# Optimization experiments

Measured on AMD Instinct MI355X. Metric: run time of the kernel, lower is better.

## Reference

```python
import jax, jax.numpy as jnp
import numpy as np

HEADS = 16
HEAD_DIM = 64
DIM = HEADS * HEAD_DIM          # 1024
TEXT_LEN = 226
N_CONCEPTS = 8
FRAMES = 4
PATCHES = 16 * 24               # H*W per latent frame
IMG_LEN = FRAMES * PATCHES      # 1536
TIME_DIM = 512
FF_DIM = 4 * DIM
TOPK_HEADS = 4                  # imap_sep_topk
LN_EPS = 1e-5
QK_EPS = 1e-6


def _layer_norm(x, w, b, eps):
    mu = jnp.mean(x, -1, keepdims=True)
    var = jnp.var(x, -1, keepdims=True)
    return (x - mu) * jax.lax.rsqrt(var + eps) * w + b


def _norm_zero(h, e, temb, lw, lb, nw, nb):
    # CogVideoXLayerNormZero: adaLN shift/scale/gate for hidden and encoder streams
    s = jax.nn.silu(temb) @ lw + lb                      # [B, 6*DIM]
    shift, scale, gate, e_shift, e_scale, e_gate = jnp.split(s, 6, axis=1)
    hn = _layer_norm(h, nw, nb, LN_EPS) * (1 + scale)[:, None] + shift[:, None]
    en = _layer_norm(e, nw, nb, LN_EPS) * (1 + e_scale)[:, None] + e_shift[:, None]
    return hn, en, gate[:, None], e_gate[:, None]


def _heads(x):
    B, S, _ = x.shape
    return x.reshape(B, S, HEADS, HEAD_DIM).transpose(0, 2, 1, 3)


def _rope(x, cos, sin):
    # diffusers apply_rotary_emb, use_real_unbind_dim=-1
    xr = x.reshape(*x.shape[:-1], HEAD_DIM // 2, 2)
    rot = jnp.stack([-xr[..., 1], xr[..., 0]], -1).reshape(x.shape)
    return x * cos + rot * sin


def _sdpa(q, k, v):
    s = jnp.einsum('bhqd,bhkd->bhqk', q, k) * (1.0 / np.sqrt(HEAD_DIM))
    return jnp.einsum('bhqk,bhkd->bhqd', jax.nn.softmax(s, -1), v)


def _attention(norm_h, norm_e, norm_c, rope_cos, rope_sin,
               wq, wk, wv, nq_w, nq_b, nk_w, nk_b, wo, bo):
    B = norm_h.shape[0]
    hs = jnp.concatenate([norm_e, norm_h], axis=1)       # [B, T+P, DIM]
    q, k, v = _heads(hs @ wq), _heads(hs @ wk), _heads(hs @ wv)
    cq, ck, cv = _heads(norm_c @ wq), _heads(norm_c @ wk), _heads(norm_c @ wv)
    q = _layer_norm(q, nq_w, nq_b, QK_EPS); cq = _layer_norm(cq, nq_w, nq_b, QK_EPS)
    k = _layer_norm(k, nk_w, nk_b, QK_EPS); ck = _layer_norm(ck, nk_w, nk_b, QK_EPS)
    q = q.at[:, :, TEXT_LEN:].set(_rope(q[:, :, TEXT_LEN:], rope_cos, rope_sin))
    k = k.at[:, :, TEXT_LEN:].set(_rope(k[:, :, TEXT_LEN:], rope_cos, rope_sin))

    attn_out = _sdpa(q, k, v)                            # [B,H,S,D]
    img_hidden = attn_out[:, :, TEXT_LEN:]               # [B,H,IMG_LEN,D]

    # select_head (reconstructed): per-head spread of image-token activations, top-k heads
    head_score = jnp.std(jnp.mean(img_hidden[1], -1), -1)        # [H]
    _, sel_head_idx = jax.lax.top_k(head_score, TOPK_HEADS)

    iq, ik, iv = q[:, :, TEXT_LEN:], k[:, :, TEXT_LEN:], v[:, :, TEXT_LEN:]
    cat_q = jnp.concatenate([cq, iq], 2)
    cat_k = jnp.concatenate([ck, ik], 2)
    cat_v = jnp.concatenate([cv, iv], 2)
    concept_attn = _sdpa(cat_q, cat_k, cat_v)
    attn_concept = concept_attn[:, :, :N_CONCEPTS]       # [B,H,C,D]

    cross_maps = jnp.mean(jnp.einsum('hpd,hcd->hcp', iq[1], ck[1]), axis=0)
    concept_maps = jnp.sum(jnp.einsum('hcd,hpd->hcp', attn_concept[1], img_hidden[1]), axis=0)

    # select_visual_token (reconstructed): per (head, concept, frame) argmax patch of q.k sim
    text_key = ck[1]                                      # imap_qk_matching_target == 'concept'
    sim = jnp.einsum('hpd,htd->htp', iq[1], text_key).reshape(HEADS, N_CONCEPTS, FRAMES, PATCHES)
    sel_vis_idx = jnp.argmax(sim, axis=-1)                # [H,T,F]

    img_r = img_hidden[1].reshape(HEADS, FRAMES, PATCHES, HEAD_DIM)
    h_ix = jnp.arange(HEADS)[:, None, None]
    f_ix = jnp.arange(FRAMES)[None, None, :]
    sel_img = img_r[h_ix, f_ix, sel_vis_idx]              # [H,T,F,D] gather
    imap = jnp.einsum('htfd,hfpd->htfp', sel_img, img_r)
    imap = (imap - imap.mean(1, keepdims=True)) / (jnp.std(imap, axis=1, keepdims=True, ddof=1) + 1e-6)
    imap = imap.reshape(HEADS, N_CONCEPTS, FRAMES * PATCHES)
    sel_imap = jnp.mean(imap[sel_head_idx], axis=0)       # [T, F*P]
    imap_sum = jnp.sum(imap, axis=0)

    def merge(x):
        return x.transpose(0, 2, 1, 3).reshape(B, x.shape[2], DIM)

    out = merge(attn_out) @ wo + bo
    c_out = merge(attn_concept) @ wo + bo
    return out[:, TEXT_LEN:], out[:, :TEXT_LEN], c_out, sel_imap, imap_sum, concept_maps, cross_maps


def _ff(x, w1, b1, w2, b2):
    return jax.nn.gelu(x @ w1 + b1, approximate=True) @ w2 + b2


def _block(hidden_states, encoder_hidden_states, concept_hidden_states, temb,
           rope_cos, rope_sin,
           norm1_w, norm1_b, ln1_w, ln1_b, norm2_w, norm2_b, ln2_w, ln2_b,
           wq, wk, wv, nq_w, nq_b, nk_w, nk_b, wo, bo,
           ff_w1, ff_b1, ff_w2, ff_b2):
    h, e, c = hidden_states, encoder_hidden_states, concept_hidden_states
    nh, ne, g_msa, eg_msa = _norm_zero(h, e, temb, norm1_w, norm1_b, ln1_w, ln1_b)
    _, nc, _, cg_msa = _norm_zero(h, c, temb, norm1_w, norm1_b, ln1_w, ln1_b)

    a_h, a_e, a_c, sel_imap, imap, concept_maps, cross_maps = _attention(
        nh, ne, nc, rope_cos, rope_sin, wq, wk, wv, nq_w, nq_b, nk_w, nk_b, wo, bo)

    h = h + g_msa * a_h
    e = e + eg_msa * a_e
    c = c + cg_msa * a_c

    nh, ne, g_ff, eg_ff = _norm_zero(h, e, temb, norm2_w, norm2_b, ln2_w, ln2_b)
    _, nc, _, cg_ff = _norm_zero(h, c, temb, norm2_w, norm2_b, ln2_w, ln2_b)

    ff_out = _ff(jnp.concatenate([ne, nh], axis=1), ff_w1, ff_b1, ff_w2, ff_b2)
    ff_c = _ff(nc, ff_w1, ff_b1, ff_w2, ff_b2)
    h = h + g_ff * ff_out[:, TEXT_LEN:]
    e = e + eg_ff * ff_out[:, :TEXT_LEN]
    c = c + cg_ff * ff_c
    return h, e, c, sel_imap, imap, concept_maps, cross_maps


def setup_inputs():
    key = jax.random.key(0)
    ks = jax.random.split(key, 16)
    p = lambda i, shape: jax.random.normal(ks[i], shape, jnp.float32) * 0.02
    return dict(
        hidden_states=jax.random.normal(ks[0], (2, IMG_LEN, DIM), jnp.float32),
        encoder_hidden_states=jax.random.normal(ks[1], (2, TEXT_LEN, DIM), jnp.float32),
        concept_hidden_states=jax.random.normal(ks[2], (2, N_CONCEPTS, DIM), jnp.float32),
        temb=jax.random.normal(ks[3], (2, TIME_DIM), jnp.float32),
        rope_cos=jax.random.uniform(ks[4], (IMG_LEN, HEAD_DIM), jnp.float32),
        rope_sin=jax.random.uniform(ks[5], (IMG_LEN, HEAD_DIM), jnp.float32),
        norm1_w=p(6, (TIME_DIM, 6 * DIM)), norm1_b=jnp.zeros((6 * DIM,), jnp.float32),
        ln1_w=jnp.ones((DIM,), jnp.float32), ln1_b=jnp.zeros((DIM,), jnp.float32),
        norm2_w=p(7, (TIME_DIM, 6 * DIM)), norm2_b=jnp.zeros((6 * DIM,), jnp.float32),
        ln2_w=jnp.ones((DIM,), jnp.float32), ln2_b=jnp.zeros((DIM,), jnp.float32),
        wq=p(8, (DIM, DIM)), wk=p(9, (DIM, DIM)), wv=p(10, (DIM, DIM)),
        nq_w=jnp.ones((HEAD_DIM,), jnp.float32), nq_b=jnp.zeros((HEAD_DIM,), jnp.float32),
        nk_w=jnp.ones((HEAD_DIM,), jnp.float32), nk_b=jnp.zeros((HEAD_DIM,), jnp.float32),
        wo=p(11, (DIM, DIM)), bo=jnp.zeros((DIM,), jnp.float32),
        ff_w1=p(12, (DIM, FF_DIM)), ff_b1=jnp.zeros((FF_DIM,), jnp.float32),
        ff_w2=p(13, (FF_DIM, DIM)), ff_b2=jnp.zeros((DIM,), jnp.float32),
    )


def reference(hidden_states, encoder_hidden_states, concept_hidden_states, temb,
              rope_cos, rope_sin,
              norm1_w, norm1_b, ln1_w, ln1_b, norm2_w, norm2_b, ln2_w, ln2_b,
              wq, wk, wv, nq_w, nq_b, nk_w, nk_b, wo, bo,
              ff_w1, ff_b1, ff_w2, ff_b2):
    return _block(hidden_states, encoder_hidden_states, concept_hidden_states, temb,
                  rope_cos, rope_sin,
                  norm1_w, norm1_b, ln1_w, ln1_b, norm2_w, norm2_b, ln2_w, ln2_b,
                  wq, wk, wv, nq_w, nq_b, nk_w, nk_b, wo, bo,
                  ff_w1, ff_b1, ff_w2, ff_b2)
```

## Files before the change

kernel.cpp:

```cpp
#include <hip/hip_runtime.h>
#include <hip/hip_bf16.h>
#include <math.h>

#define B_ 2
#define HEADS_ 16
#define HD_ 64
#define DIM_ 1024
#define TEXT_ 226
#define NC_ 8
#define FRAMES_ 4
#define PATCHES_ 384
#define IMG_ 1536
#define S_MAIN 1762
#define S2_ 1770
#define TD_ 512
#define FF_ 4096
#define ROWS_ (B_*S2_)
#define VPAD_ 1792

#define OFF_S1   0L
#define OFF_S2   12288L
#define OFF_MISC 24576L
#define OFF_SIM  25600L
#define OFF_IMAP 222208L
#define OFF_AC   418816L
#define OFF_X    435200L
#define OFF_PROJ 4060160L
#define OFF_XN   7685120L
#define OFF_Q    11310080L
#define OFF_K    14935040L
#define OFF_V    18560000L
#define OFF_AO   22184960L
#define OFF_XNB  25809920L

#define O_H    0L
#define O_E    3145728L
#define O_C    3608576L
#define O_SELI 3624960L
#define O_ISUM 3637248L
#define O_CMAP 3649536L
#define O_XMAP 3661824L

typedef __bf16 bf16x8_t __attribute__((ext_vector_type(8)));
typedef float  f32x4_t  __attribute__((ext_vector_type(4)));

__device__ __forceinline__ unsigned int pack2bf(float a, float b) {
    unsigned short ua = __builtin_bit_cast(unsigned short, (__bf16)a);
    unsigned short ub = __builtin_bit_cast(unsigned short, (__bf16)b);
    return (unsigned int)ua | ((unsigned int)ub << 16);
}

__global__ __launch_bounds__(256) void k_silu_mod(
    const float* __restrict__ temb, const float* __restrict__ w1, const float* __restrict__ b1,
    const float* __restrict__ w2, const float* __restrict__ b2,
    float* __restrict__ s1, float* __restrict__ s2)
{
    int gout = blockIdx.x * 64 + (threadIdx.x & 63);
    int ks = threadIdx.x >> 6;
    int which = gout / 12288;
    int r = gout % 12288;
    int b = r / 6144, n = r % 6144;
    const float* w = which ? w2 : w1;
    const float* bb = which ? b2 : b1;
    const float* t = temb + b * TD_;
    float acc = 0.f;
    for (int k = ks*128; k < ks*128 + 128; ++k) {
        float tv = t[k];
        float sv = tv / (1.f + __expf(-tv));
        acc += sv * w[(long)k * 6144 + n];
    }
    __shared__ float red[256];
    red[threadIdx.x] = acc; __syncthreads();
    if (ks == 0) {
        int lt = threadIdx.x;
        float v = red[lt] + red[lt+64] + red[lt+128] + red[lt+192] + bb[n];
        (which ? s2 : s1)[b * 6144 + n] = v;
    }
}

__global__ __launch_bounds__(256) void k_tcvt(
    const float* __restrict__ src, unsigned short* __restrict__ dst, int K, int N)
{
    __shared__ float t[32][33];
    int n0 = blockIdx.x * 32, k0 = blockIdx.y * 32;
    int tx = threadIdx.x & 31, ty = threadIdx.x >> 5;
    #pragma unroll
    for (int i = 0; i < 4; ++i)
        t[ty + 8*i][tx] = src[(size_t)(k0 + ty + 8*i) * N + n0 + tx];
    __syncthreads();
    #pragma unroll
    for (int i = 0; i < 4; ++i) {
        float v = t[tx][ty + 8*i];
        dst[(size_t)(n0 + ty + 8*i) * K + k0 + tx] =
            __builtin_bit_cast(unsigned short, (__bf16)v);
    }
}

__global__ __launch_bounds__(256) void k_tcvt_qkv(
    const float* __restrict__ wq, const float* __restrict__ wk, const float* __restrict__ wv,
    unsigned short* __restrict__ dst)
{
    const float* src = (blockIdx.z == 0) ? wq : (blockIdx.z == 1) ? wk : wv;
    unsigned short* d = dst + (size_t)blockIdx.z * 1024 * 1024;
    __shared__ float t[32][33];
    int n0 = blockIdx.x * 32, k0 = blockIdx.y * 32;
    int tx = threadIdx.x & 31, ty = threadIdx.x >> 5;
    #pragma unroll
    for (int i = 0; i < 4; ++i)
        t[ty + 8*i][tx] = src[(size_t)(k0 + ty + 8*i) * 1024 + n0 + tx];
    __syncthreads();
    #pragma unroll
    for (int i = 0; i < 4; ++i) {
        float v = t[tx][ty + 8*i];
        d[(size_t)(n0 + ty + 8*i) * 1024 + k0 + tx] =
            __builtin_bit_cast(unsigned short, (__bf16)v);
    }
}

__global__ __launch_bounds__(256) void k_vtrans(
    const float* __restrict__ vh, unsigned short* __restrict__ vb)
{
    int bh = blockIdx.z;
    int d0 = blockIdx.y * 32;
    int s0 = blockIdx.x * 32;
    __shared__ float t[32][33];
    int tx = threadIdx.x & 31, ty = threadIdx.x >> 5;
    const float* src = vh + (size_t)bh * S2_ * 64;
    #pragma unroll
    for (int i = 0; i < 4; ++i) {
        int s = s0 + ty + 8*i; if (s >= S2_) s = S2_ - 1;
        t[ty + 8*i][tx] = src[(size_t)s*64 + d0 + tx];
    }
    __syncthreads();
    unsigned short* dst = vb + (size_t)bh * 64 * VPAD_;
    #pragma unroll
    for (int i = 0; i < 4; ++i) {
        int d = d0 + ty + 8*i;
        dst[(size_t)d * VPAD_ + s0 + tx] =
            __builtin_bit_cast(unsigned short, (__bf16)t[tx][ty + 8*i]);
    }
}

__global__ __launch_bounds__(256) void k_ln_mod(
    const float* pe, long bse, const float* ph, long bsh, const float* pc, long bsc,
    const float* __restrict__ smod, const float* __restrict__ lnw, const float* __restrict__ lnb,
    float* __restrict__ out, unsigned short* __restrict__ outb)
{
    long row = blockIdx.x;
    int b = (int)(row / S2_), s = (int)(row % S2_);
    const float* src; int shiftB, scaleB;
    if (s < TEXT_)       { src = pe + (long)b*bse + (long)s*DIM_;          shiftB = 3072; scaleB = 4096; }
    else if (s < S_MAIN) { src = ph + (long)b*bsh + (long)(s-TEXT_)*DIM_;  shiftB = 0;    scaleB = 1024; }
    else                 { src = pc + (long)b*bsc + (long)(s-S_MAIN)*DIM_; shiftB = 3072; scaleB = 4096; }
    int tid = threadIdx.x;
    int col = tid * 4;
    float4 x = *(const float4*)(src + col);
    float lsum = x.x + x.y + x.z + x.w;
    float lsq  = x.x*x.x + x.y*x.y + x.z*x.z + x.w*x.w;
    __shared__ float r1[256], r2[256];
    r1[tid] = lsum; r2[tid] = lsq; __syncthreads();
    for (int st = 128; st; st >>= 1) {
        if (tid < st) { r1[tid] += r1[tid+st]; r2[tid] += r2[tid+st]; }
        __syncthreads();
    }
    float mu = r1[0] * (1.f / DIM_);
    float var = r2[0] * (1.f / DIM_) - mu * mu;
    float rstd = rsqrtf(var + 1e-5f);
    const float* sb = smod + (long)b * 6144;
    float xs[4] = {x.x, x.y, x.z, x.w};
    float res[4];
    #pragma unroll
    for (int i = 0; i < 4; ++i) {
        int cc = col + i;
        float yy = (xs[i] - mu) * rstd * lnw[cc] + lnb[cc];
        res[i] = yy * (1.f + sb[scaleB + cc]) + sb[shiftB + cc];
    }
    if (out)
        *(float4*)(out + row * DIM_ + col) = make_float4(res[0], res[1], res[2], res[3]);
    uint2 pk;
    pk.x = pack2bf(res[0], res[1]); pk.y = pack2bf(res[2], res[3]);
    *(uint2*)(outb + row * DIM_ + col) = pk;
}

__global__ __launch_bounds__(256, 3) void k_bgemm(
    const unsigned short* __restrict__ A, const unsigned short* __restrict__ Wt,
    const float* __restrict__ bias, float* __restrict__ out_f,
    unsigned short* __restrict__ out_b, int M, int N, int K, int kz_len, int mode,
    float* __restrict__ q_out, float* __restrict__ k_out, float* __restrict__ v_out)
{
    __shared__ unsigned short at[2][128*40];
    __shared__ unsigned short bt[2][128*40];
    int tid = threadIdx.x;
    int w = tid >> 6, lane = tid & 63;
    int lr = lane & 15, lh = lane >> 4;
    int wm = w >> 1, wn = w & 1;
    int m0 = blockIdx.y * 128, n0 = blockIdx.x * 128;
    int kbeg = blockIdx.z * kz_len, kend = kbeg + kz_len;

    f32x4_t acc[4][4];
    #pragma unroll
    for (int i = 0; i < 4; ++i)
        #pragma unroll
        for (int j = 0; j < 4; ++j) { acc[i][j][0]=0.f; acc[i][j][1]=0.f; acc[i][j][2]=0.f; acc[i][j][3]=0.f; }

    int srow = tid >> 1, shalf = tid & 1;
    int arow = m0 + srow; if (arow >= M) arow = M - 1;
    const unsigned short* aptr = A + (size_t)arow * K + shalf * 16;
    const unsigned short* bptr = Wt + (size_t)(n0 + srow) * K + shalf * 16;
    int soff = srow * 40 + shalf * 16;

    {
        int4 a0 = *(const int4*)(aptr + kbeg);
        int4 a1 = *(const int4*)(aptr + kbeg + 8);
        int4 b0 = *(const int4*)(bptr + kbeg);
        int4 b1 = *(const int4*)(bptr + kbeg + 8);
        *(int4*)&at[0][soff] = a0; *(int4*)&at[0][soff + 8] = a1;
        *(int4*)&bt[0][soff] = b0; *(int4*)&bt[0][soff + 8] = b1;
    }
    __syncthreads();
    int buf = 0;
    for (int k0 = kbeg; k0 < kend; k0 += 32) {
        bool more = (k0 + 32) < kend;
        int4 na0, na1, nb0, nb1;
        if (more) {
            na0 = *(const int4*)(aptr + k0 + 32);
            na1 = *(const int4*)(aptr + k0 + 40);
            nb0 = *(const int4*)(bptr + k0 + 32);
            nb1 = *(const int4*)(bptr + k0 + 40);
        }
        int4 af[4], bf[4];
        #pragma unroll
        for (int tm = 0; tm < 4; ++tm)
            af[tm] = *(const int4*)&at[buf][(wm*64 + tm*16 + lr)*40 + lh*8];
        #pragma unroll
        for (int tn = 0; tn < 4; ++tn)
            bf[tn] = *(const int4*)&bt[buf][(wn*64 + tn*16 + lr)*40 + lh*8];
        #pragma unroll
        for (int tm = 0; tm < 4; ++tm) {
            bf16x8_t av = __builtin_bit_cast(bf16x8_t, af[tm]);
            #pragma unroll
            for (int tn = 0; tn < 4; ++tn)
                acc[tm][tn] = __builtin_amdgcn_mfma_f32_16x16x32_bf16(
                    av, __builtin_bit_cast(bf16x8_t, bf[tn]), acc[tm][tn], 0, 0, 0);
        }
        if (more) {
            int nb = buf ^ 1;
            *(int4*)&at[nb][soff] = na0; *(int4*)&at[nb][soff + 8] = na1;
            *(int4*)&bt[nb][soff] = nb0; *(int4*)&bt[nb][soff + 8] = nb1;
            __syncthreads();
            buf = nb;
        }
    }
    float* of = out_f;
    if (mode == 1) of += (size_t)blockIdx.z * M * N;
    #pragma unroll
    for (int tm = 0; tm < 4; ++tm) {
        #pragma unroll
        for (int r = 0; r < 4; ++r) {
            int m = m0 + wm*64 + tm*16 + lh*4 + r;
            if (m >= M) continue;
            int b = m / S2_, s = m % S2_;
            #pragma unroll
            for (int tn = 0; tn < 4; ++tn) {
                int n = n0 + wn*64 + tn*16 + lr;
                float v = acc[tm][tn][r];
                if (mode == 0) {
                    int which = n >> 10, c = n & 1023;
                    int hh = c >> 6, d = c & 63;
                    float* dstp = (which == 0) ? q_out : (which == 1) ? k_out : v_out;
                    dstp[(((size_t)b*HEADS_ + hh)*S2_ + s)*64 + d] = v;
                } else if (mode == 1) {
                    of[(size_t)m * N + n] = v + (bias ? bias[n] : 0.f);
                } else {
                    float x = v + bias[n];
                    float u = 0.7978845608028654f * (x + 0.044715f*x*x*x);
                    float g = x / (1.f + __expf(-2.f*u));
                    out_b[(size_t)m * N + n] = __builtin_bit_cast(unsigned short, (__bf16)g);
                }
            }
        }
    }
}

__global__ __launch_bounds__(256) void k_gemm(
    const float* __restrict__ A, const float* __restrict__ W,
    float* __restrict__ C, int M, int N, int K, int kz_len, int headed, int row_off,
    float* __restrict__ part)
{
    __shared__ float As[16][68];
    __shared__ float Bs[16][68];
    int tid = threadIdx.x;
    int bm = blockIdx.y * 64, bn = blockIdx.x * 64;
    int tr = tid >> 4, tc = tid & 15;
    int ar = tid >> 2, akk = (tid & 3) * 4;
    int bkk = tid >> 4, bn4 = (tid & 15) * 4;
    float acc[4][4] = {{0.f}};
    int garow = bm + ar;
    const float* Aptr = A + (size_t)garow * K + akk;
    const float* Wptr = W + (size_t)bkk * N + bn + bn4;
    int kbeg = blockIdx.z * kz_len;
    for (int k0 = kbeg; k0 < kbeg + kz_len; k0 += 16) {
        float4 av = make_float4(0.f, 0.f, 0.f, 0.f);
        if (garow < M) av = *(const float4*)(Aptr + k0);
        As[akk+0][ar] = av.x; As[akk+1][ar] = av.y; As[akk+2][ar] = av.z; As[akk+3][ar] = av.w;
        float4 bv = *(const float4*)(Wptr + (size_t)k0 * N);
        Bs[bkk][bn4+0] = bv.x; Bs[bkk][bn4+1] = bv.y; Bs[bkk][bn4+2] = bv.z; Bs[bkk][bn4+3] = bv.w;
        __syncthreads();
        #pragma unroll
        for (int kk = 0; kk < 16; ++kk) {
            float4 a = *(const float4*)&As[kk][tr*4];
            float4 bq = *(const float4*)&Bs[kk][tc*4];
            float avv[4] = {a.x, a.y, a.z, a.w};
            float bvv[4] = {bq.x, bq.y, bq.z, bq.w};
            #pragma unroll
            for (int i = 0; i < 4; ++i)
                #pragma unroll
                for (int j = 0; j < 4; ++j)
                    acc[i][j] += avv[i] * bvv[j];
        }
        __syncthreads();
    }
    #pragma unroll
    for (int i = 0; i < 4; ++i) {
        int r = bm + tr*4 + i;
        if (r >= M) continue;
        #pragma unroll
        for (int j = 0; j < 4; ++j) {
            int n = bn + tc*4 + j;
            float v = acc[i][j];
            if (part) {
                part[(size_t)blockIdx.z*M*N + (size_t)r*N + n] = v;
            } else if (headed) {
                int rg = r + row_off;
                int b = rg / S2_, s = rg % S2_;
                int hh = n >> 6, d = n & 63;
                C[(((size_t)b*HEADS_ + hh)*S2_ + s)*64 + d] = v;
            } else {
                C[(size_t)(r + row_off) * N + n] = v;
            }
        }
    }
}

__global__ __launch_bounds__(256) void k_fixred(
    const float* __restrict__ pa, float* __restrict__ qh_out)
{
    long i = (long)blockIdx.x*256 + threadIdx.x;
    int r = (int)(i >> 10), n = (int)(i & 1023);
    float v = pa[i] + pa[i + (long)IMG_*DIM_];
    int hh = n >> 6, d = n & 63;
    qh_out[(((size_t)HEADS_ + hh)*S2_ + TEXT_ + r)*64 + d] = v;
}

__global__ __launch_bounds__(256) void k_qk_prep(
    float* qh, float* kh, unsigned short* qbb, unsigned short* kbb,
    const float* __restrict__ nqw, const float* __restrict__ nqb,
    const float* __restrict__ nkw, const float* __restrict__ nkb,
    const float* __restrict__ rc, const float* __restrict__ rs)
{
    int which = blockIdx.y;
    int wid = threadIdx.x >> 6;
    int lane = threadIdx.x & 63;
    long row = (long)blockIdx.x * 4 + wid;
    long s = row % S2_;
    bool b1 = row >= (long)HEADS_*S2_;
    float* base = (which ? kh : qh) + row * 64;
    const float* w  = which ? nkw : nqw;
    const float* bb = which ? nkb : nqb;
    float x = base[lane];
    float sum = x;
    for (int off = 1; off < 64; off <<= 1) sum += __shfl_xor(sum, off, 64);
    float mu = sum * (1.f / 64.f);
    float dx = x - mu;
    float v = dx * dx;
    for (int off = 1; off < 64; off <<= 1) v += __shfl_xor(v, off, 64);
    float rstd = rsqrtf(v * (1.f / 64.f) + 1e-6f);
    float y = dx * rstd * w[lane] + bb[lane];
    if (s >= TEXT_ && s < S_MAIN) {
        long p = s - TEXT_;
        float part = __shfl_xor(y, 1, 64);
        float rot = (lane & 1) ? part : -part;
        y = y * rc[p*64 + lane] + rot * rs[p*64 + lane];
    }
    bool needf = b1 && (which ? (s >= S_MAIN) : (s >= TEXT_ && s < S_MAIN));
    if (needf) base[lane] = y;
    (which ? kbb : qbb)[row * 64 + lane] = __builtin_bit_cast(unsigned short, (__bf16)y);
}

__global__ __launch_bounds__(256) void k_flash(
    const unsigned short* __restrict__ qb, const unsigned short* __restrict__ kb,
    const unsigned short* __restrict__ vb,
    float* __restrict__ p0, float* __restrict__ p1, float* __restrict__ pl)
{
    int bx = blockIdx.x;
    int h = blockIdx.y, b = blockIdx.z;
    int qt, NQ, q_off, r0s, r0e, r1s, r1e, z;
    if (bx < 28) {
        z = bx & 1; int u = bx >> 1;
        qt = u*128; NQ = S_MAIN; q_off = 0;
        r0s = z ? 896 : 0; r0e = z ? S_MAIN : 896;
        r1s = 0; r1e = 0;
    } else {
        z = bx - 28;
        qt = 0; NQ = NC_; q_off = S_MAIN;
        if (z == 0) { r0s = S_MAIN;      r0e = S2_;    r1s = TEXT_; r1e = TEXT_ + 768; }
        else        { r0s = TEXT_ + 768; r0e = S_MAIN; r1s = 0;     r1e = 0; }
    }
    float* po = z ? p1 : p0;
    int tid = threadIdx.x;
    int w = tid >> 6, lane = tid & 63;
    int lr = lane & 15, lh = lane >> 4;
    __shared__ __align__(16) unsigned short kt[64*72];
    __shared__ __align__(16) unsigned short vt[64*72];
    __shared__ __align__(16) unsigned short pbuf[4*32*72];
    unsigned short* pw = pbuf + w*32*72;
    const unsigned short* qbase = qb + (((size_t)b*HEADS_ + h)*S2_ + q_off)*64;
    const unsigned short* kbase = kb + ((size_t)b*HEADS_ + h)*S2_*64;
    const unsigned short* vbase = vb + (size_t)(b*HEADS_ + h)*64*VPAD_;
    bf16x8_t aq[2][2];
    #pragma unroll
    for (int t = 0; t < 2; ++t) {
        int qrow = qt + w*32 + t*16 + lr; if (qrow >= NQ) qrow = NQ - 1;
        const unsigned short* qsrc = qbase + (size_t)qrow*64 + lh*8;
        aq[t][0] = __builtin_bit_cast(bf16x8_t, *(const int4*)qsrc);
        aq[t][1] = __builtin_bit_cast(bf16x8_t, *(const int4*)(qsrc + 32));
    }
    int4 onesi = make_int4(0x3F803F80, 0x3F803F80, 0x3F803F80, 0x3F803F80);
    bf16x8_t bones = __builtin_bit_cast(bf16x8_t, onesi);
    f32x4_t O[2][4];
    f32x4_t Lacc[2];
    #pragma unroll
    for (int t = 0; t < 2; ++t) {
        Lacc[t][0]=0.f; Lacc[t][1]=0.f; Lacc[t][2]=0.f; Lacc[t][3]=0.f;
        #pragma unroll
        for (int g = 0; g < 4; ++g) { O[t][g][0]=0.f; O[t][g][1]=0.f; O[t][g][2]=0.f; O[t][g][3]=0.f; }
    }
    for (int rgi = 0; rgi < 2; ++rgi) {
        int rs = rgi ? r1s : r0s, re = rgi ? r1e : r0e;
        for (int j0 = rs; j0 < re; j0 += 64) {
            int cnt = min(64, re - j0);
            __syncthreads();
            #pragma unroll
            for (int i = 0; i < 2; ++i) {
                int idx = tid + i*256;
                int key = idx >> 3, p8 = idx & 7;
                int krow = j0 + key; if (krow > re - 1) krow = re - 1;
                *(int4*)&kt[key*72 + p8*8] = *(const int4*)(kbase + (size_t)krow*64 + p8*8);
            }
            #pragma unroll
            for (int i = 0; i < 2; ++i) {
                int idx = tid + i*256;
                int d = idx >> 3, p8 = idx & 7;
                *(int4*)&vt[d*72 + p8*8] = *(const int4*)(vbase + (size_t)d*VPAD_ + j0 + p8*8);
            }
            __syncthreads();
            f32x4_t S[2][4];
            #pragma unroll
            for (int g = 0; g < 4; ++g) {
                const unsigned short* kr = &kt[(16*g + lr)*72 + lh*8];
                bf16x8_t b0 = __builtin_bit_cast(bf16x8_t, *(const int4*)kr);
                bf16x8_t b1 = __builtin_bit_cast(bf16x8_t, *(const int4*)(kr + 32));
                #pragma unroll
                for (int t = 0; t < 2; ++t) {
                    f32x4_t zz; zz[0]=0.f; zz[1]=0.f; zz[2]=0.f; zz[3]=0.f;
                    zz = __builtin_amdgcn_mfma_f32_16x16x32_bf16(aq[t][0], b0, zz, 0, 0, 0);
                    zz = __builtin_amdgcn_mfma_f32_16x16x32_bf16(aq[t][1], b1, zz, 0, 0, 0);
                    S[t][g] = zz;
                }
            }
            #pragma unroll
            for (int t = 0; t < 2; ++t)
                #pragma unroll
                for (int g = 0; g < 4; ++g) {
                    bool vld = (16*g + lr) < cnt;
                    #pragma unroll
                    for (int r = 0; r < 4; ++r) {
                        float p = vld ? __expf(S[t][g][r] * 0.125f) : 0.f;
                        pw[(t*16 + lh*4 + r)*72 + 16*g + lr] = __builtin_bit_cast(unsigned short, (__bf16)p);
                    }
                }
            #pragma unroll
            for (int c = 0; c < 2; ++c) {
                bf16x8_t ap[2];
                #pragma unroll
                for (int t = 0; t < 2; ++t) {
                    ap[t] = __builtin_bit_cast(bf16x8_t,
                        *(const int4*)&pw[(t*16 + lr)*72 + c*32 + lh*8]);
                    Lacc[t] = __builtin_amdgcn_mfma_f32_16x16x32_bf16(ap[t], bones, Lacc[t], 0, 0, 0);
                }
                #pragma unroll
                for (int g = 0; g < 4; ++g) {
                    bf16x8_t bv = __builtin_bit_cast(bf16x8_t,
                        *(const int4*)&vt[(16*g + lr)*72 + c*32 + lh*8]);
                    #pragma unroll
                    for (int t = 0; t < 2; ++t)
                        O[t][g] = __builtin_amdgcn_mfma_f32_16x16x32_bf16(ap[t], bv, O[t][g], 0, 0, 0);
                }
            }
        }
    }
    #pragma unroll
    for (int t = 0; t < 2; ++t)
        #pragma unroll
        for (int r = 0; r < 4; ++r) {
            int gq = qt + w*32 + t*16 + lh*4 + r;
            if (gq < NQ) {
                long rrow = (long)(b*HEADS_ + h)*S2_ + q_off + gq;
                float* o = po + rrow*64 + lr;
                #pragma unroll
                for (int g = 0; g < 4; ++g) o[16*g] = O[t][g][r];
                if (lr == 0) pl[(long)z*(B_*HEADS_*S2_) + rrow] = Lacc[t][r];
            }
        }
}

__global__ __launch_bounds__(256) void k_fcomb(
    const float* __restrict__ p0, const float* __restrict__ p1,
    const float* __restrict__ pl,
    float* __restrict__ ao, float* __restrict__ ac)
{
    long i = (long)blockIdx.x*256 + threadIdx.x;
    int d = (int)(i & 63);
    long rrow = i >> 6;
    int s = (int)(rrow % S2_);
    int bh = (int)(rrow / S2_);
    float l = pl[rrow] + pl[rrow + (long)B_*HEADS_*S2_];
    float v = (p0[i] + p1[i]) / l;
    if (s < S_MAIN) ao[((long)bh*S_MAIN + s)*64 + d] = v;
    else            ac[((long)bh*NC_ + (s - S_MAIN))*64 + d] = v;
}

__global__ __launch_bounds__(256) void k_head_score(const float* __restrict__ ao, float* __restrict__ score)
{
    int h = blockIdx.x, tid = threadIdx.x;
    const float* base = ao + (((long)HEADS_ + h)*S_MAIN + TEXT_)*64;
    float sA = 0.f, sB = 0.f;
    for (int p = tid; p < IMG_; p += 256) {
        const float* r = base + (long)p*64;
        float mm = 0.f;
        for (int d = 0; d < 64; d += 4) {
            float4 v = *(const float4*)(r + d);
            mm += v.x + v.y + v.z + v.w;
        }
        mm *= (1.f / 64.f);
        sA += mm; sB += mm*mm;
    }
    __shared__ float r1[256], r2[256];
    r1[tid] = sA; r2[tid] = sB; __syncthreads();
    for (int st = 128; st; st >>= 1) {
        if (tid < st) { r1[tid] += r1[tid+st]; r2[tid] += r2[tid+st]; }
        __syncthreads();
    }
    if (tid == 0) {
        float mean = r1[0] / IMG_, ms = r2[0] / IMG_;
        score[h] = sqrtf(fmaxf(ms - mean*mean, 0.f));
    }
}

__global__ void k_top4(const float* __restrict__ score, int* __restrict__ sel)
{
    if (threadIdx.x == 0 && blockIdx.x == 0) {
        int used = 0;
        for (int k = 0; k < 4; ++k) {
            float best = -INFINITY; int bi = 0;
            for (int h2 = 0; h2 < 16; ++h2) {
                if (used & (1 << h2)) continue;
                if (score[h2] > best) { best = score[h2]; bi = h2; }
            }
            used |= 1 << bi; sel[k] = bi;
        }
    }
}

__global__ __launch_bounds__(512) void k_sim(
    const float* __restrict__ qh, const float* __restrict__ kh,
    float* __restrict__ sim, int* __restrict__ selvis)
{
    int blk = blockIdx.x;
    int h = blk >> 5, t = (blk >> 2) & 7, f = blk & 3;
    int tid = threadIdx.x;
    __shared__ float ckv[64];
    if (tid < 64) ckv[tid] = kh[(((long)HEADS_ + h)*S2_ + S_MAIN + t)*64 + tid];
    __syncthreads();
    float val = -INFINITY; int idx = 0x7fffffff;
    if (tid < PATCHES_) {
        const float* qrow = qh + (((long)HEADS_ + h)*S2_ + TEXT_ + f*PATCHES_ + tid)*64;
        float acc = 0.f;
        for (int d = 0; d < 64; d += 4) {
            float4 qv = *(const float4*)(qrow + d);
            acc += qv.x*ckv[d] + qv.y*ckv[d+1] + qv.z*ckv[d+2] + qv.w*ckv[d+3];
        }
        sim[((long)h*NC_ + t)*IMG_ + f*PATCHES_ + tid] = acc;
        val = acc; idx = tid;
    }
    __shared__ float sv[512]; __shared__ int si[512];
    sv[tid] = val; si[tid] = idx; __syncthreads();
    for (int st = 256; st; st >>= 1) {
        if (tid < st) {
            float v2 = sv[tid+st]; int i2 = si[tid+st];
            if (v2 > sv[tid] || (v2 == sv[tid] && i2 < si[tid])) { sv[tid] = v2; si[tid] = i2; }
        }
        __syncthreads();
    }
    if (tid == 0) selvis[blk] = si[0];
}

__global__ __launch_bounds__(256) void k_cross(const float* __restrict__ sim, float* __restrict__ out)
{
    int i = blockIdx.x*256 + threadIdx.x;
    int c = i / IMG_, p = i % IMG_;
    float acc = 0.f;
    for (int h = 0; h < 16; ++h) acc += sim[((long)h*NC_ + c)*IMG_ + p];
    out[O_XMAP + i] = acc * (1.f / 16.f);
}

__global__ __launch_bounds__(256) void k_concept_maps(
    const float* __restrict__ ac, const float* __restrict__ ao, float* __restrict__ out)
{
    int i = blockIdx.x*256 + threadIdx.x;
    int c = i / IMG_, p = i % IMG_;
    float acc = 0.f;
    for (int h = 0; h < 16; ++h) {
        const float* a = ac + (((long)HEADS_ + h)*NC_ + c)*64;
        const float* g = ao + (((long)HEADS_ + h)*S_MAIN + TEXT_ + p)*64;
        for (int d = 0; d < 64; d += 4) {
            float4 av = *(const float4*)(a + d);
            float4 gv = *(const float4*)(g + d);
            acc += av.x*gv.x + av.y*gv.y + av.z*gv.z + av.w*gv.w;
        }
    }
    out[O_CMAP + i] = acc;
}

__global__ void k_imap_raw(const float* __restrict__ ao, const int* __restrict__ selvis,
                           float* __restrict__ imap)
{
    int blk = blockIdx.x;
    int h = blk >> 5, t = (blk >> 2) & 7, f = blk & 3;
    int tid = threadIdx.x;
    __shared__ float sel[64];
    int pstar = selvis[blk];
    if (tid < 64) sel[tid] = ao[(((long)HEADS_ + h)*S_MAIN + TEXT_ + f*PATCHES_ + pstar)*64 + tid];
    __syncthreads();
    const float* g = ao + (((long)HEADS_ + h)*S_MAIN + TEXT_ + f*PATCHES_ + tid)*64;
    float acc = 0.f;
    for (int d = 0; d < 64; d += 4) {
        float4 gv = *(const float4*)(g + d);
        acc += gv.x*sel[d] + gv.y*sel[d+1] + gv.z*sel[d+2] + gv.w*sel[d+3];
    }
    imap[((long)h*NC_ + t)*IMG_ + f*PATCHES_ + tid] = acc;
}

__global__ __launch_bounds__(256) void k_imap_norm(float* __restrict__ imap)
{
    int i = blockIdx.x*256 + threadIdx.x;
    int h = i / IMG_, fp = i % IMG_;
    float v[8]; float mu = 0.f;
    #pragma unroll
    for (int t = 0; t < 8; ++t) { v[t] = imap[((long)h*NC_ + t)*IMG_ + fp]; mu += v[t]; }
    mu *= 0.125f;
    float var = 0.f;
    #pragma unroll
    for (int t = 0; t < 8; ++t) var += (v[t]-mu)*(v[t]-mu);
    float sd = sqrtf(var * (1.f / 7.f));
    float inv = 1.f / (sd + 1e-6f);
    #pragma unroll
    for (int t = 0; t < 8; ++t) imap[((long)h*NC_ + t)*IMG_ + fp] = (v[t]-mu)*inv;
}

__global__ __launch_bounds__(256) void k_imap_reduce(
    const float* __restrict__ imap, const int* __restrict__ sel, float* __restrict__ out)
{
    int i = blockIdx.x*256 + threadIdx.x;
    int t = i / IMG_, fp = i % IMG_;
    float sum = 0.f;
    for (int h = 0; h < 16; ++h) sum += imap[((long)h*NC_ + t)*IMG_ + fp];
    float ss = 0.f;
    for (int k = 0; k < 4; ++k) { int h = sel[k]; ss += imap[((long)h*NC_ + t)*IMG_ + fp]; }
    out[O_ISUM + i] = sum;
    out[O_SELI + i] = ss * 0.25f;
}

__global__ __launch_bounds__(256) void k_merge(
    const float* __restrict__ ao, const float* __restrict__ ac, unsigned short* __restrict__ xo)
{
    long i = (long)blockIdx.x*256 + threadIdx.x;
    int col = (int)(i & 1023);
    long row = i >> 10;
    int b = (int)(row / S2_), s = (int)(row % S2_);
    int h = col >> 6, d = col & 63;
    float v;
    if (s < S_MAIN) v = ao[(((long)b*HEADS_ + h)*S_MAIN + s)*64 + d];
    else            v = ac[(((long)b*HEADS_ + h)*NC_ + (s - S_MAIN))*64 + d];
    xo[i] = __builtin_bit_cast(unsigned short, (__bf16)v);
}

__global__ __launch_bounds__(256) void k_residual1(
    const float* __restrict__ pe, const float* __restrict__ ph, const float* __restrict__ pc,
    const float* __restrict__ p0, const float* __restrict__ p1, const float* __restrict__ bo,
    const float* __restrict__ s1, float* __restrict__ X)
{
    long i = (long)blockIdx.x*256 + threadIdx.x;
    int col = (int)(i & 1023);
    long row = i >> 10;
    int b = (int)(row / S2_), s = (int)(row % S2_);
    const float* sb = s1 + (long)b * 6144;
    float orig, gate;
    if (s < TEXT_)       { orig = pe[((long)b*TEXT_ + s)*DIM_ + col];            gate = sb[5120 + col]; }
    else if (s < S_MAIN) { orig = ph[((long)b*IMG_ + (s-TEXT_))*DIM_ + col];     gate = sb[2048 + col]; }
    else                 { orig = pc[((long)b*NC_ + (s-S_MAIN))*DIM_ + col];     gate = sb[5120 + col]; }
    X[i] = orig + gate * (p0[i] + p1[i] + bo[col]);
}

__global__ __launch_bounds__(256) void k_final(
    const float* __restrict__ X, const float* __restrict__ f0, const float* __restrict__ f1,
    const float* __restrict__ fb2, const float* __restrict__ s2, float* __restrict__ out)
{
    long i = (long)blockIdx.x*256 + threadIdx.x;
    int col = (int)(i & 1023);
    long row = i >> 10;
    int b = (int)(row / S2_), s = (int)(row % S2_);
    const float* sb = s2 + (long)b * 6144;
    float gate; float* o;
    if (s < TEXT_)       { gate = sb[5120 + col]; o = out + O_E + ((long)b*TEXT_ + s)*DIM_ + col; }
    else if (s < S_MAIN) { gate = sb[2048 + col]; o = out + O_H + ((long)b*IMG_ + (s-TEXT_))*DIM_ + col; }
    else                 { gate = sb[5120 + col]; o = out + O_C + ((long)b*NC_ + (s-S_MAIN))*DIM_ + col; }
    *o = X[i] + gate * (f0[i] + f1[i] + fb2[col]);
}

extern "C" void kernel_launch(void* const* d_in, const int* in_sizes, int n_in,
                              void* d_out, int out_size, void* d_ws, size_t ws_size,
                              hipStream_t stream)
{
    (void)in_sizes; (void)n_in; (void)out_size; (void)ws_size;
    const float* h_in = (const float*)d_in[0];
    const float* e_in = (const float*)d_in[1];
    const float* c_in = (const float*)d_in[2];
    const float* temb = (const float*)d_in[3];
    const float* rcos = (const float*)d_in[4];
    const float* rsin = (const float*)d_in[5];
    const float* n1w  = (const float*)d_in[6];
    const float* n1b  = (const float*)d_in[7];
    const float* ln1w = (const float*)d_in[8];
    const float* ln1b = (const float*)d_in[9];
    const float* n2w  = (const float*)d_in[10];
    const float* n2b  = (const float*)d_in[11];
    const float* ln2w = (const float*)d_in[12];
    const float* ln2b = (const float*)d_in[13];
    const float* wq   = (const float*)d_in[14];
    const float* wk   = (const float*)d_in[15];
    const float* wv   = (const float*)d_in[16];
    const float* nqw  = (const float*)d_in[17];
    const float* nqb  = (const float*)d_in[18];
    const float* nkw  = (const float*)d_in[19];
    const float* nkb  = (const float*)d_in[20];
    const float* wo   = (const float*)d_in[21];
    const float* bo   = (const float*)d_in[22];
    const float* fw1  = (const float*)d_in[23];
    const float* fb1  = (const float*)d_in[24];
    const float* fw2  = (const float*)d_in[25];
    const float* fb2  = (const float*)d_in[26];

    float* ws  = (float*)d_ws;
    float* out = (float*)d_out;
    float* s1   = ws + OFF_S1;
    float* s2   = ws + OFF_S2;
    float* score  = ws + OFF_MISC;
    int*   selh   = (int*)(ws + OFF_MISC + 16);
    int*   selvis = (int*)(ws + OFF_MISC + 32);
    float* sim  = ws + OFF_SIM;
    float* imap = ws + OFF_IMAP;
    float* ac   = ws + OFF_AC;
    float* X    = ws + OFF_X;
    float* proj = ws + OFF_PROJ;
    float* xn   = ws + OFF_XN;
    float* qh   = ws + OFF_Q;
    float* kh   = ws + OFF_K;
    float* vh   = ws + OFF_V;
    float* ao   = ws + OFF_AO;
    float* ffo  = proj;
    float* fixp = ws + OFF_AO;
    unsigned short* xnb   = (unsigned short*)(ws + OFF_XNB);
    unsigned short* wqkvT = (unsigned short*)(ws + OFF_PROJ);
    unsigned short* vb    = (unsigned short*)(ws + OFF_PROJ);
    unsigned short* qbb   = (unsigned short*)(ws + OFF_X);
    unsigned short* kbb   = qbb + (size_t)B_*HEADS_*S2_*64;
    unsigned short* woT   = (unsigned short*)(ws + OFF_AO + 2000000);
    unsigned short* fw1T  = (unsigned short*)(ws + OFF_V);
    unsigned short* fw2T  = (unsigned short*)(ws + OFF_AO);
    unsigned short* ffh   = (unsigned short*)(ws + OFF_Q);
    float* fp0 = vh;
    float* fp1 = xn;
    float* fpl = sim;

    hipLaunchKernelGGL(k_silu_mod, dim3(384), dim3(256), 0, stream, temb, n1w, n1b, n2w, n2b, s1, s2);
    hipLaunchKernelGGL(k_tcvt_qkv, dim3(32, 32, 3), dim3(256), 0, stream, wq, wk, wv, wqkvT);
    hipLaunchKernelGGL(k_ln_mod, dim3(ROWS_), dim3(256), 0, stream,
        e_in, (long)TEXT_*DIM_, h_in, (long)IMG_*DIM_, c_in, (long)NC_*DIM_, s1, ln1w, ln1b, xn, xnb);
    hipLaunchKernelGGL(k_bgemm, dim3(24, 28, 1), dim3(256), 0, stream,
        xnb, wqkvT, (const float*)nullptr, (float*)nullptr, (unsigned short*)nullptr,
        ROWS_, 3072, 1024, 1024, 0, qh, kh, vh);
    hipLaunchKernelGGL(k_gemm, dim3(16, 24, 2), dim3(256), 0, stream,
        xn + (long)(S2_ + TEXT_)*DIM_, wq, (float*)nullptr, IMG_, DIM_, DIM_, 512, 0, 0, fixp);
    hipLaunchKernelGGL(k_fixred, dim3(6144), dim3(256), 0, stream, fixp, qh);
    hipLaunchKernelGGL(k_gemm, dim3(16, 1, 1), dim3(256), 0, stream,
        xn + (long)(S2_ + S_MAIN)*DIM_, wk, kh, NC_, DIM_, DIM_, 1024, 1, S2_ + S_MAIN, (float*)nullptr);
    hipLaunchKernelGGL(k_qk_prep, dim3(14160, 2), dim3(256), 0, stream,
        qh, kh, qbb, kbb, nqw, nqb, nkw, nkb, rcos, rsin);
    hipLaunchKernelGGL(k_vtrans, dim3(56, 2, 32), dim3(256), 0, stream, vh, vb);
    hipLaunchKernelGGL(k_flash, dim3(30, 16, 2), dim3(256), 0, stream,
        qbb, kbb, vb, fp0, fp1, fpl);
    hipLaunchKernelGGL(k_fcomb, dim3(14160), dim3(256), 0, stream, fp0, fp1, fpl, ao, ac);
    hipLaunchKernelGGL(k_head_score, dim3(16), dim3(256), 0, stream, ao, score);
    hipLaunchKernelGGL(k_top4, dim3(1), dim3(64), 0, stream, score, selh);
    hipLaunchKernelGGL(k_sim, dim3(512), dim3(512), 0, stream, qh, kh, sim, selvis);
    hipLaunchKernelGGL(k_cross, dim3(48), dim3(256), 0, stream, sim, out);
    hipLaunchKernelGGL(k_concept_maps, dim3(48), dim3(256), 0, stream, ac, ao, out);
    hipLaunchKernelGGL(k_imap_raw, dim3(512), dim3(384), 0, stream, ao, selvis, imap);
    hipLaunchKernelGGL(k_imap_norm, dim3(96), dim3(256), 0, stream, imap);
    hipLaunchKernelGGL(k_imap_reduce, dim3(48), dim3(256), 0, stream, imap, selh, out);
    hipLaunchKernelGGL(k_merge, dim3(14160), dim3(256), 0, stream, ao, ac, xnb);
    hipLaunchKernelGGL(k_tcvt, dim3(32, 32), dim3(256), 0, stream, wo, woT, 1024, 1024);
    hipLaunchKernelGGL(k_bgemm, dim3(8, 28, 2), dim3(256), 0, stream,
        xnb, woT, (const float*)nullptr, proj, (unsigned short*)nullptr, ROWS_, DIM_, 1024, 512, 1,
        (float*)nullptr, (float*)nullptr, (float*)nullptr);
    hipLaunchKernelGGL(k_residual1, dim3(14160), dim3(256), 0, stream,
        e_in, h_in, c_in, proj, proj + (size_t)ROWS_*DIM_, bo, s1, X);
    hipLaunchKernelGGL(k_tcvt, dim3(128, 32), dim3(256), 0, stream, fw1, fw1T, 1024, 4096);
    hipLaunchKernelGGL(k_tcvt, dim3(32, 128), dim3(256), 0, stream, fw2, fw2T, 4096, 1024);
    hipLaunchKernelGGL(k_ln_mod, dim3(ROWS_), dim3(256), 0, stream,
        X, (long)S2_*DIM_, X + (long)TEXT_*DIM_, (long)S2_*DIM_, X + (long)S_MAIN*DIM_, (long)S2_*DIM_,
        s2, ln2w, ln2b, (float*)nullptr, xnb);
    hipLaunchKernelGGL(k_bgemm, dim3(32, 28, 1), dim3(256), 0, stream,
        xnb, fw1T, fb1, (float*)nullptr, ffh, ROWS_, FF_, 1024, 1024, 2,
        (float*)nullptr, (float*)nullptr, (float*)nullptr);
    hipLaunchKernelGGL(k_bgemm, dim3(8, 28, 2), dim3(256), 0, stream,
        ffh, fw2T, (const float*)nullptr, ffo, (unsigned short*)nullptr, ROWS_, DIM_, FF_, 2048, 1,
        (float*)nullptr, (float*)nullptr, (float*)nullptr);
    hipLaunchKernelGGL(k_final, dim3(14160), dim3(256), 0, stream,
        X, ffo, ffo + (size_t)ROWS_*DIM_, fb2, s2, out);
}
```

Baseline: 745.8 us.

## Stage GEMM tiles directly from global to LDS and raise occupancy

```diff
diff --git a/kernel.cpp b/kernel.cpp
--- a/kernel.cpp
+++ b/kernel.cpp
@@ -48,6 +48,12 @@
     unsigned short ua = __builtin_bit_cast(unsigned short, (__bf16)a);
     unsigned short ub = __builtin_bit_cast(unsigned short, (__bf16)b);
     return (unsigned int)ua | ((unsigned int)ub << 16);
+}
+
+__device__ __forceinline__ void stage16(const unsigned short* g, unsigned short* l) {
+    __builtin_amdgcn_global_load_lds(
+        (const __attribute__((address_space(1))) unsigned int*)g,
+        (__attribute__((address_space(3))) unsigned int*)l, 16, 0, 0);
 }
 
 __global__ __launch_bounds__(256) void k_silu_mod(
@@ -182,14 +188,14 @@
     *(uint2*)(outb + row * DIM_ + col) = pk;
 }
 
-__global__ __launch_bounds__(256, 3) void k_bgemm(
+__global__ __launch_bounds__(256, 4) void k_bgemm(
     const unsigned short* __restrict__ A, const unsigned short* __restrict__ Wt,
     const float* __restrict__ bias, float* __restrict__ out_f,
     unsigned short* __restrict__ out_b, int M, int N, int K, int kz_len, int mode,
     float* __restrict__ q_out, float* __restrict__ k_out, float* __restrict__ v_out)
 {
-    __shared__ unsigned short at[2][128*40];
-    __shared__ unsigned short bt[2][128*40];
+    __shared__ unsigned short at[2][128*32];
+    __shared__ unsigned short bt[2][128*32];
     int tid = threadIdx.x;
     int w = tid >> 6, lane = tid & 63;
     int lr = lane & 15, lh = lane >> 4;
@@ -203,38 +209,37 @@
         #pragma unroll
         for (int j = 0; j < 4; ++j) { acc[i][j][0]=0.f; acc[i][j][1]=0.f; acc[i][j][2]=0.f; acc[i][j][3]=0.f; }
 
-    int srow = tid >> 1, shalf = tid & 1;
-    int arow = m0 + srow; if (arow >= M) arow = M - 1;
-    const unsigned short* aptr = A + (size_t)arow * K + shalf * 16;
-    const unsigned short* bptr = Wt + (size_t)(n0 + srow) * K + shalf * 16;
-    int soff = srow * 40 + shalf * 16;
-
-    {
-        int4 a0 = *(const int4*)(aptr + kbeg);
-        int4 a1 = *(const int4*)(aptr + kbeg + 8);
-        int4 b0 = *(const int4*)(bptr + kbeg);
-        int4 b1 = *(const int4*)(bptr + kbeg + 8);
-        *(int4*)&at[0][soff] = a0; *(int4*)&at[0][soff + 8] = a1;
-        *(int4*)&bt[0][soff] = b0; *(int4*)&bt[0][soff + 8] = b1;
-    }
+    int r4 = tid >> 2, c4 = tid & 3;
+    int arow0 = m0 + r4;      if (arow0 >= M) arow0 = M - 1;
+    int arow1 = m0 + 64 + r4; if (arow1 >= M) arow1 = M - 1;
+    const unsigned short* ga0 = A + (size_t)arow0 * K + c4 * 8;
+    const unsigned short* ga1 = A + (size_t)arow1 * K + c4 * 8;
+    const unsigned short* gb0 = Wt + (size_t)(n0 + r4) * K + c4 * 8;
+    const unsigned short* gb1 = Wt + (size_t)(n0 + 64 + r4) * K + c4 * 8;
+    int lbase = w * 512;
+
+    stage16(ga0 + kbeg, &at[0][lbase]);
+    stage16(ga1 + kbeg, &at[0][lbase + 2048]);
+    stage16(gb0 + kbeg, &bt[0][lbase]);
+    stage16(gb1 + kbeg, &bt[0][lbase + 2048]);
     __syncthreads();
     int buf = 0;
     for (int k0 = kbeg; k0 < kend; k0 += 32) {
         bool more = (k0 + 32) < kend;
-        int4 na0, na1, nb0, nb1;
         if (more) {
-            na0 = *(const int4*)(aptr + k0 + 32);
-            na1 = *(const int4*)(aptr + k0 + 40);
-            nb0 = *(const int4*)(bptr + k0 + 32);
-            nb1 = *(const int4*)(bptr + k0 + 40);
+            int nb = buf ^ 1;
+            stage16(ga0 + k0 + 32, &at[nb][lbase]);
+            stage16(ga1 + k0 + 32, &at[nb][lbase + 2048]);
+            stage16(gb0 + k0 + 32, &bt[nb][lbase]);
+            stage16(gb1 + k0 + 32, &bt[nb][lbase + 2048]);
         }
         int4 af[4], bf[4];
         #pragma unroll
         for (int tm = 0; tm < 4; ++tm)
-            af[tm] = *(const int4*)&at[buf][(wm*64 + tm*16 + lr)*40 + lh*8];
+            af[tm] = *(const int4*)&at[buf][(wm*64 + tm*16 + lr)*32 + lh*8];
         #pragma unroll
         for (int tn = 0; tn < 4; ++tn)
-            bf[tn] = *(const int4*)&bt[buf][(wn*64 + tn*16 + lr)*40 + lh*8];
+            bf[tn] = *(const int4*)&bt[buf][(wn*64 + tn*16 + lr)*32 + lh*8];
         #pragma unroll
         for (int tm = 0; tm < 4; ++tm) {
             bf16x8_t av = __builtin_bit_cast(bf16x8_t, af[tm]);
@@ -243,13 +248,8 @@
                 acc[tm][tn] = __builtin_amdgcn_mfma_f32_16x16x32_bf16(
                     av, __builtin_bit_cast(bf16x8_t, bf[tn]), acc[tm][tn], 0, 0, 0);
         }
-        if (more) {
-            int nb = buf ^ 1;
-            *(int4*)&at[nb][soff] = na0; *(int4*)&at[nb][soff + 8] = na1;
-            *(int4*)&bt[nb][soff] = nb0; *(int4*)&bt[nb][soff + 8] = nb1;
-            __syncthreads();
-            buf = nb;
-        }
+        __syncthreads();
+        buf ^= 1;
     }
     float* of = out_f;
     if (mode == 1) of += (size_t)blockIdx.z * M * N;
```

Result: no change. 734.4 us (-1.5%).
